# Optimization experiments

Hardware: AMD Instinct MI355X
Metric: run time of the kernel (lower is better)

## Reference

```python
import jax, jax.numpy as jnp
import numpy as np

N = 50000       # nodes
E = 800000      # edges (avg degree 16)
IN_DIM = 64
H = 64          # hidden_dim
OUT_DIM = 64
R = 8           # n_relations
L = 3           # n_layers
LN_EPS = 1e-5
NEG_SLOPE = 0.2


def _layer_norm(x, g, b):
    mu = jnp.mean(x, axis=-1, keepdims=True)
    var = jnp.mean((x - mu) ** 2, axis=-1, keepdims=True)
    return (x - mu) * jax.lax.rsqrt(var + LN_EPS) * g + b


def setup_inputs() -> dict:
    key = jax.random.key(0)
    ks = jax.random.split(key, 10)
    s = 0.05
    return {
        "x": jax.random.normal(ks[0], (N, IN_DIM), jnp.float32),
        "edge_index": jax.random.randint(ks[1], (2, E), 0, N),
        "edge_type": jax.random.randint(ks[2], (E,), 0, R),
        "W_in": jax.random.normal(ks[3], (H, IN_DIM), jnp.float32) * s,
        "b_in": jnp.zeros((H,), jnp.float32),
        "W_rel": jax.random.normal(ks[4], (R, H, H), jnp.float32) * s,   # no bias
        "W_gate": jax.random.normal(ks[5], (R, H, H), jnp.float32) * s,
        "b_gate": jnp.zeros((R, H), jnp.float32),
        "W_att": jax.random.normal(ks[6], (R, 2 * H), jnp.float32) * s,  # Linear(2H,1) per relation
        "b_att": jnp.zeros((R,), jnp.float32),
        "ln_gamma": jnp.ones((L, H), jnp.float32),
        "ln_beta": jnp.zeros((L, H), jnp.float32),
        "W_out": jax.random.normal(ks[7], (OUT_DIM, H), jnp.float32) * s,
        "b_out": jnp.zeros((OUT_DIM,), jnp.float32),
    }


def reference(x, edge_index, edge_type, W_in, b_in, W_rel, W_gate, b_gate,
              W_att, b_att, ln_gamma, ln_beta, W_out, b_out):
    src, dst = edge_index[0], edge_index[1]
    Wa_src, Wa_dst = W_att[:, :H], W_att[:, H:]      # [R,H] each
    seg = dst * R + edge_type                        # combined (node, relation) scatter key
    eidx = jnp.arange(E)

    h = jax.nn.relu(x @ W_in.T + b_in)               # [N,H]

    for layer in range(L):
        h_src = h[src]                               # [E,H] gather
        h_dst = h[dst]                               # [E,H] gather
        # attention score of each edge under its own relation's Linear(2H,1)
        scores_all = h_src @ Wa_src.T + h_dst @ Wa_dst.T + b_att   # [E,R]
        scores = scores_all[eidx, edge_type]                        # [E]
        scores = jax.nn.leaky_relu(scores, NEG_SLOPE)
        # softmax over dim=0 within each relation's edge set (as in the torch code)
        m = jax.ops.segment_max(scores, edge_type, num_segments=R)
        ex = jnp.exp(scores - m[edge_type])
        denom = jax.ops.segment_sum(ex, edge_type, num_segments=R)
        att = ex / denom[edge_type]                                 # [E]
        # relation-specific linear of source features (linear commutes with gather)
        hWr = jnp.einsum('nh,rkh->nrk', h, W_rel)                   # [N,R,H]
        msg = hWr[src, edge_type] * att[:, None]                    # [E,H]
        # per-relation scatter-add into destinations
        agg = jax.ops.segment_sum(msg, seg, num_segments=N * R)     # [N*R,H]
        agg = agg.reshape(N, R, H)
        gate = jax.nn.sigmoid(jnp.einsum('nh,rkh->nrk', h, W_gate) + b_gate)  # [N,R,H]
        h_new = jnp.mean(gate * agg, axis=1)         # sum(messages)/n_relations
        h = jax.nn.relu(_layer_norm(h + h_new, ln_gamma[layer], ln_beta[layer]))

    return h @ W_out.T + b_out
```

## Files before the change

### kernel.cpp

```cpp
#include <hip/hip_runtime.h>
#include <math.h>

#define NN 50000
#define EE 800000
#define HH 64
#define RR 8
#define LL 3
#define NR (NN * RR)
#define NB ((NR + 255) / 256)
#define LN_EPS 1e-5f
#define NEG_SLOPE 0.2f
#define LDH 68
#define OTB (16 * LDH)
#define DSPREAD 64
#define NPB 80
#define NGRP 5

typedef __attribute__((ext_vector_type(8))) short bf8;
typedef __attribute__((ext_vector_type(4))) float f4;
typedef __attribute__((ext_vector_type(2))) float f2;
typedef __attribute__((ext_vector_type(8))) unsigned short us8;
typedef __attribute__((ext_vector_type(2))) unsigned int u2;
typedef __attribute__((ext_vector_type(4))) unsigned int u4;

#define WLOADP(d0, d1, sbase, vbyte) \
    asm volatile("global_load_dwordx4 %0, %2, %3 offset:0\n\t" \
                 "global_load_dwordx4 %1, %2, %3 offset:64" \
        : "=&v"(d0), "=&v"(d1) : "v"(vbyte), "s"(sbase) : "memory")

__device__ __forceinline__ unsigned short bf16r(float f) {
    unsigned u = __float_as_uint(f);
    unsigned r = u + 0x7fffu + ((u >> 16) & 1u);
    return (unsigned short)(r >> 16);
}
__device__ __forceinline__ float bf2f(unsigned short u) {
    return __uint_as_float(((unsigned)u) << 16);
}
__device__ __forceinline__ bf8 asbf8(u4 v) {
    union { u4 a; bf8 b; } c; c.a = v; return c.b;
}
__device__ __forceinline__ void stage16(const void* g, void* l) {
    __builtin_amdgcn_global_load_lds(
        (const __attribute__((address_space(1))) void*)g,
        (__attribute__((address_space(3))) void*)l, 16, 0, 0);
}

__global__ __launch_bounds__(256) void proj_in(
    const float* __restrict__ x, const float* __restrict__ W,
    const float* __restrict__ bias, const unsigned short* __restrict__ WaB,
    float* __restrict__ h, unsigned short* __restrict__ hbf,
    float* __restrict__ s_src, float* __restrict__ s_dst) {
    __shared__ float WT[64 * LDH];
    __shared__ float xs[16 * LDH];
    __shared__ float hs[16 * LDH];
    int tid = threadIdx.x;
    int n0 = blockIdx.x * 16;
    #pragma unroll
    for (int s = 0; s < 16; ++s) {
        int idx = tid + 256 * s;
        int k = idx >> 6, i = idx & 63;
        WT[i * LDH + k] = W[idx];
    }
    int row = tid >> 4, cg = tid & 15;
    {
        f4 v = ((const f4*)x)[(size_t)(n0 + row) * 16 + cg];
        *(f4*)&xs[row * LDH + cg * 4] = v;
    }
    __syncthreads();
    f4 acc;
    {
        f4 b = *(const f4*)(bias + cg * 4);
        acc = b;
        #pragma unroll
        for (int i = 0; i < 64; ++i) {
            float xv = xs[row * LDH + i];
            f4 wt = *(const f4*)&WT[i * LDH + cg * 4];
            acc[0] += xv * wt[0];
            acc[1] += xv * wt[1];
            acc[2] += xv * wt[2];
            acc[3] += xv * wt[3];
        }
        #pragma unroll
        for (int j = 0; j < 4; ++j) acc[j] = fmaxf(acc[j], 0.f);
        int n = n0 + row;
        *(f4*)(h + (size_t)n * 64 + cg * 4) = acc;
        u2 u;
        u[0] = (unsigned)bf16r(acc[0]) | ((unsigned)bf16r(acc[1]) << 16);
        u[1] = (unsigned)bf16r(acc[2]) | ((unsigned)bf16r(acc[3]) << 16);
        *(u2*)(hbf + (size_t)n * 64 + cg * 4) = u;
        *(f4*)&hs[row * LDH + cg * 4] = acc;
    }
    __syncthreads();
    if (tid < 64) {
        int lane = tid;
        int quad = lane >> 4, lr = lane & 15;
        f4 sc = (f4){0.f, 0.f, 0.f, 0.f};
        #pragma unroll
        for (int kb = 0; kb < 2; ++kb) {
            const float* p = &hs[lr * LDH + kb * 32 + quad * 8];
            bf8 a;
            #pragma unroll
            for (int j = 0; j < 8; ++j) a[j] = (short)bf16r(p[j]);
            const bf8* bw = (const bf8*)(WaB + lr * 64 + kb * 32 + quad * 8);
            sc = __builtin_amdgcn_mfma_f32_16x16x32_bf16(a, *bw, sc, 0, 0, 0);
        }
        #pragma unroll
        for (int j = 0; j < 4; ++j) {
            int n = n0 + quad * 4 + j;
            if (lr < 8) s_src[n * 8 + lr] = sc[j];
            else        s_dst[n * 8 + (lr - 8)] = sc[j];
        }
    }
}

__global__ void edge_count(const int* __restrict__ ei, const int* __restrict__ et,
                           int* __restrict__ counts, int* __restrict__ rank) {
    int e = blockIdx.x * 256 + threadIdx.x;
    int d = ei[EE + e], t = et[e];
    rank[e] = atomicAdd(&counts[d * 8 + t], 1);
}

__global__ void scan1(const int* __restrict__ counts, int* __restrict__ offs,
                      int* __restrict__ bsum) {
    __shared__ int s[256];
    int tid = threadIdx.x;
    int i = blockIdx.x * 256 + tid;
    int v = (i < NR) ? counts[i] : 0;
    s[tid] = v; __syncthreads();
    for (int d = 1; d < 256; d <<= 1) {
        int x = (tid >= d) ? s[tid - d] : 0;
        __syncthreads();
        s[tid] += x;
        __syncthreads();
    }
    if (i < NR) offs[i] = s[tid] - v;
    if (tid == 255) bsum[blockIdx.x] = s[255];
}

__global__ void scan2(int* __restrict__ bsum) {
    __shared__ int s[1024];
    int tid = threadIdx.x;
    int carry = 0;
    for (int c0 = 0; c0 < NB; c0 += 1024) {
        int i = c0 + tid;
        int v = (i < NB) ? bsum[i] : 0;
        s[tid] = v; __syncthreads();
        for (int d = 1; d < 1024; d <<= 1) {
            int x = (tid >= d) ? s[tid - d] : 0;
            __syncthreads();
            s[tid] += x;
            __syncthreads();
        }
        if (i < NB) bsum[i] = carry + s[tid] - v;
        int tot = s[1023];
        __syncthreads();
        carry += tot;
    }
}

__global__ void edge_fill(const int* __restrict__ ei, const int* __restrict__ et,
                          const int* __restrict__ rank, const int* __restrict__ offs,
                          const int* __restrict__ bsum, u2* __restrict__ spack) {
    int e = blockIdx.x * 256 + threadIdx.x;
    int s = ei[e], d = ei[EE + e], t = et[e];
    int seg = d * 8 + t;
    int slot = offs[seg] + bsum[seg >> 8] + rank[e];
    spack[slot] = (u2){(unsigned)s, (unsigned)seg};
}

__global__ void cvt_w(const float* __restrict__ Wr, const float* __restrict__ Wg,
                      const float* __restrict__ Wa, const float* __restrict__ Wo,
                      unsigned short* __restrict__ WrB, unsigned short* __restrict__ WgB,
                      unsigned short* __restrict__ WaB, unsigned short* __restrict__ WoB) {
    int i = blockIdx.x * 256 + threadIdx.x;
    WrB[i] = bf16r(Wr[i]);
    WgB[i] = bf16r(Wg[i]);
    if (i < 1024) {
        int row = i >> 6, k = i & 63;
        float v = (row < 8) ? Wa[row * 128 + k] : Wa[(row - 8) * 128 + 64 + k];
        WaB[i] = bf16r(v);
    }
    if (i < 4096) WoB[i] = bf16r(Wo[i]);
}

__global__ void edge_softmax2(const u2* __restrict__ spack,
                              const float* __restrict__ s_src, const float* __restrict__ s_dst,
                              const float* __restrict__ b_att,
                              u2* __restrict__ epack, float* __restrict__ dpart) {
    __shared__ float lsum[4][8];
    int tid = threadIdx.x;
    if (tid < 32) lsum[tid >> 3][tid & 7] = 0.f;
    __syncthreads();
    int slot = blockIdx.x * 256 + tid;
    u2 sp = spack[slot];
    int src = (int)sp[0];
    int seg = (int)sp[1];
    int t = seg & 7;
    float sc = s_src[src * 8 + t] + s_dst[seg] + b_att[t];
    sc = (sc >= 0.f) ? sc : NEG_SLOPE * sc;
    float ex = __expf(sc);
    epack[slot] = (u2){(unsigned)src, __float_as_uint(ex)};
    atomicAdd(&lsum[tid >> 6][t], ex);
    __syncthreads();
    if (tid < 8) {
        float v = lsum[0][tid] + lsum[1][tid] + lsum[2][tid] + lsum[3][tid];
        atomicAdd(&dpart[(blockIdx.x & (DSPREAD - 1)) * 16 + tid], v);
    }
}

__global__ void denom_reduce(const float* __restrict__ dpartL,
                             float* __restrict__ idn8L) {
    __shared__ float sb[256];
    int t = threadIdx.x;
    int rb = t >> 3, ty = t & 7;
    float v = dpartL[rb * 16 + ty] + dpartL[(rb + 32) * 16 + ty];
    sb[t] = v; __syncthreads();
    for (int st = 128; st >= 8; st >>= 1) {
        if (t < st) sb[t] += sb[t + st];
        __syncthreads();
    }
    if (t < 8) idn8L[t] = 1.f / sb[t];
}

__global__ __launch_bounds__(256, 4) void gather_seg(
    const int* __restrict__ offs, const int* __restrict__ bsum,
    const u2* __restrict__ epack, const float* __restrict__ idn8L,
    const unsigned short* __restrict__ hbf_in,
    unsigned short* __restrict__ psG) {
    int tid = threadIdx.x;
    int segl = tid >> 1, half = tid & 1;
    int sidx = blockIdx.x * 128 + segl;
    int lo = offs[sidx] + bsum[sidx >> 8];
    int nxt = sidx + 1;
    int hi = (nxt < NR) ? (offs[nxt] + bsum[nxt >> 8]) : EE;
    int r = segl & 7, gn = segl >> 3;

    f4 d0 = *(const f4*)(idn8L);
    f4 d1 = *(const f4*)(idn8L + 4);
    float i01 = (r & 1) ? d0[1] : d0[0];
    float i23 = (r & 1) ? d0[3] : d0[2];
    float i45 = (r & 1) ? d1[1] : d1[0];
    float i67 = (r & 1) ? d1[3] : d1[2];
    float i03 = (r & 2) ? i23 : i01;
    float i47 = (r & 2) ? i67 : i45;
    float idn = (r & 4) ? i47 : i03;

    f2 acc[16];
    #pragma unroll
    for (int i = 0; i < 16; ++i) acc[i] = (f2){0.f, 0.f};

    for (int s = lo; s < hi; s += 4) {
        int i1 = (s + 1 < hi) ? s + 1 : s;
        int i2 = (s + 2 < hi) ? s + 2 : s;
        int i3 = (s + 3 < hi) ? s + 3 : s;
        u2 pk0 = epack[s], pk1 = epack[i1], pk2 = epack[i2], pk3 = epack[i3];
        float a0 = __uint_as_float(pk0[1]);
        float a1 = (s + 1 < hi) ? __uint_as_float(pk1[1]) : 0.f;
        float a2 = (s + 2 < hi) ? __uint_as_float(pk2[1]) : 0.f;
        float a3 = (s + 3 < hi) ? __uint_as_float(pk3[1]) : 0.f;
        const u4* hp0 = (const u4*)(hbf_in + ((size_t)(int)pk0[0] << 6) + half * 32);
        const u4* hp1 = (const u4*)(hbf_in + ((size_t)(int)pk1[0] << 6) + half * 32);
        const u4* hp2 = (const u4*)(hbf_in + ((size_t)(int)pk2[0] << 6) + half * 32);
        const u4* hp3 = (const u4*)(hbf_in + ((size_t)(int)pk3[0] << 6) + half * 32);
        #pragma unroll
        for (int q = 0; q < 4; ++q) {
            u4 v0 = hp0[q], v1 = hp1[q], v2 = hp2[q], v3 = hp3[q];
            #pragma unroll
            for (int k = 0; k < 4; ++k) {
                f2 w0, w1, w2, w3;
                w0[0] = __uint_as_float(v0[k] << 16);
                w0[1] = __uint_as_float(v0[k] & 0xffff0000u);
                w1[0] = __uint_as_float(v1[k] << 16);
                w1[1] = __uint_as_float(v1[k] & 0xffff0000u);
                w2[0] = __uint_as_float(v2[k] << 16);
                w2[1] = __uint_as_float(v2[k] & 0xffff0000u);
                w3[0] = __uint_as_float(v3[k] << 16);
                w3[1] = __uint_as_float(v3[k] & 0xffff0000u);
                acc[q * 4 + k] += (f2){a0, a0} * w0;
                acc[q * 4 + k] += (f2){a1, a1} * w1;
                acc[q * 4 + k] += (f2){a2, a2} * w2;
                acc[q * 4 + k] += (f2){a3, a3} * w3;
            }
        }
    }

    unsigned short* base = psG + ((size_t)blockIdx.x << 13) + gn * 512 + r * 64;
    #pragma unroll
    for (int q = 0; q < 4; ++q) {
        us8 o;
        #pragma unroll
        for (int k = 0; k < 4; ++k) {
            o[2 * k]     = bf16r(acc[q * 4 + k][0] * idn);
            o[2 * k + 1] = bf16r(acc[q * 4 + k][1] * idn);
        }
        int c2 = (half * 4 + q) ^ (gn & 7);
        *(us8*)(base + c2 * 8) = o;
    }
}

#define STAGE_GRP(b, g) do { \
    int n0s_ = nb0 + (g) * 16; \
    const char* ps_src_ = (const char*)psG + (size_t)n0s_ * 1024; \
    _Pragma("unroll") \
    for (int i_ = 0; i_ < 4; ++i_) { \
        unsigned off_ = i_ * 4096 + w * 1024; \
        stage16(ps_src_ + off_ + lane * 16, (char*)psL[b] + off_); \
    } \
    unsigned a_ = (unsigned)(w * 1024 + lane * 16); \
    unsigned sa_ = a_ ^ (((a_ >> 8) & 7u) << 4); \
    stage16((const char*)(hbuf + (size_t)n0s_ * 64) + sa_, (char*)hsL[b] + a_); \
} while (0)

template<bool EMIT, bool OUT>
__global__ __launch_bounds__(256, 2) void combine_dense(
    const float* __restrict__ hbuf, const unsigned short* __restrict__ psG,
    const unsigned short* __restrict__ WrB, const unsigned short* __restrict__ WgB,
    const unsigned short* __restrict__ WaB, const unsigned short* __restrict__ WoB,
    const float* __restrict__ b_gate, const float* __restrict__ gamma,
    const float* __restrict__ beta, float* __restrict__ hout,
    unsigned short* __restrict__ hbf_out, float* __restrict__ ssrc_out,
    float* __restrict__ sdst_out, float* __restrict__ outp,
    const float* __restrict__ b_out) {
    __shared__ unsigned short psL[2][8192];
    __shared__ float hsL[2][1024];
    int tid = threadIdx.x;
    int nb0 = blockIdx.x * NPB;
    int w = tid >> 6, lane = tid & 63;
    int quad = lane >> 4, lr = lane & 15;
    int tn = w;

    STAGE_GRP(0, 0);

    unsigned rowb = (unsigned)((tn * 16 + lr) * 128 + quad * 16);
    u4 wr[8][2], wg[8][2];
    #pragma unroll
    for (int r = 0; r < 8; ++r) {
        WLOADP(wr[r][0], wr[r][1], WrB, rowb + (unsigned)r * 8192u);
        WLOADP(wg[r][0], wg[r][1], WgB, rowb + (unsigned)r * 8192u);
    }
    float bgv[8];
    #pragma unroll
    for (int r = 0; r < 8; ++r) bgv[r] = b_gate[r * 64 + tn * 16 + lr];
    f4 gmv = *(const f4*)(gamma + (tid & 15) * 4);
    f4 btv = *(const f4*)(beta + (tid & 15) * 4);

    for (int g = 0; g < NGRP; ++g) {
        int cb = g & 1;
        int n0 = nb0 + g * 16;
        if (g + 1 < NGRP) {
            STAGE_GRP(cb ^ 1, g + 1);
            asm volatile("s_waitcnt vmcnt(5)" ::: "memory");
        } else {
            asm volatile("s_waitcnt vmcnt(0)" ::: "memory");
        }
        __builtin_amdgcn_sched_barrier(0);
        __builtin_amdgcn_s_barrier();

        bf8 a_h[2];
        #pragma unroll
        for (int kb = 0; kb < 2; ++kb) {
            unsigned c0 = (unsigned)(kb * 8 + quad * 2)     ^ (unsigned)(lr & 7);
            unsigned c1 = (unsigned)(kb * 8 + quad * 2 + 1) ^ (unsigned)(lr & 7);
            f4 p0 = *(const f4*)((const char*)hsL[cb] + lr * 256 + c0 * 16);
            f4 p1 = *(const f4*)((const char*)hsL[cb] + lr * 256 + c1 * 16);
            bf8 a;
            #pragma unroll
            for (int j = 0; j < 4; ++j) a[j] = (short)bf16r(p0[j]);
            #pragma unroll
            for (int j = 0; j < 4; ++j) a[4 + j] = (short)bf16r(p1[j]);
            a_h[kb] = a;
        }

        f4 acc = (f4){0.f, 0.f, 0.f, 0.f};
        #pragma unroll
        for (int r = 0; r < 8; ++r) {
            bf8 a_p[2];
            #pragma unroll
            for (int kb = 0; kb < 2; ++kb) {
                unsigned c = (unsigned)(kb * 4 + quad) ^ (unsigned)(lr & 7);
                a_p[kb] = *(const bf8*)((const char*)psL[cb] + lr * 1024 + r * 128 + c * 16);
            }
            f4 aggc = (f4){0.f, 0.f, 0.f, 0.f};
            f4 gacc = (f4){0.f, 0.f, 0.f, 0.f};
            aggc = __builtin_amdgcn_mfma_f32_16x16x32_bf16(a_p[0], asbf8(wr[r][0]), aggc, 0, 0, 0);
            gacc = __builtin_amdgcn_mfma_f32_16x16x32_bf16(a_h[0], asbf8(wg[r][0]), gacc, 0, 0, 0);
            aggc = __builtin_amdgcn_mfma_f32_16x16x32_bf16(a_p[1], asbf8(wr[r][1]), aggc, 0, 0, 0);
            gacc = __builtin_amdgcn_mfma_f32_16x16x32_bf16(a_h[1], asbf8(wg[r][1]), gacc, 0, 0, 0);
            #pragma unroll
            for (int j = 0; j < 4; ++j) {
                float gt = 1.f / (1.f + __expf(-(gacc[j] + bgv[r])));
                acc[j] += gt * aggc[j];
            }
        }
        __syncthreads();

        float* ps_f = (float*)psL[cb];
        #pragma unroll
        for (int j = 0; j < 4; ++j) {
            int row = quad * 4 + j;
            int col = tn * 16 + lr;
            unsigned y = (unsigned)(row * 256 + col * 4);
            float hres = *(const float*)((const char*)hsL[cb] + (y ^ (((unsigned)(row & 7)) << 4)));
            ps_f[row * LDH + col] = hres + acc[j] * 0.125f;
        }
        __syncthreads();

        {
            int row = tid >> 4, c = tid & 15;
            int n = n0 + row;
            f4 tv = *(const f4*)&ps_f[row * LDH + c * 4];
            float s1 = tv[0] + tv[1] + tv[2] + tv[3];
            float s2 = tv[0]*tv[0] + tv[1]*tv[1] + tv[2]*tv[2] + tv[3]*tv[3];
            #pragma unroll
            for (int off = 1; off <= 8; off <<= 1) {
                s1 += __shfl_xor(s1, off, 64);
                s2 += __shfl_xor(s2, off, 64);
            }
            float mu = s1 * (1.f / 64.f);
            float var = s2 * (1.f / 64.f) - mu * mu;
            float rs = rsqrtf(var + LN_EPS);
            f4 ov;
            #pragma unroll
            for (int j = 0; j < 4; ++j)
                ov[j] = fmaxf((tv[j] - mu) * rs * gmv[j] + btv[j], 0.f);
            if (!OUT)
                *(f4*)(hout + (size_t)n * 64 + c * 4) = ov;
            *(f4*)&ps_f[OTB + row * LDH + c * 4] = ov;
            if (EMIT) {
                u2 u;
                u[0] = (unsigned)bf16r(ov[0]) | ((unsigned)bf16r(ov[1]) << 16);
                u[1] = (unsigned)bf16r(ov[2]) | ((unsigned)bf16r(ov[3]) << 16);
                *(u2*)(hbf_out + (size_t)n * 64 + c * 4) = u;
            }
        }

        if (EMIT) {
            __syncthreads();
            if (w == 0) {
                f4 sc = (f4){0.f, 0.f, 0.f, 0.f};
                #pragma unroll
                for (int kb = 0; kb < 2; ++kb) {
                    const float* p = &ps_f[OTB + lr * LDH + kb * 32 + quad * 8];
                    bf8 a;
                    #pragma unroll
                    for (int j = 0; j < 8; ++j) a[j] = (short)bf16r(p[j]);
                    const bf8* bw = (const bf8*)(WaB + lr * 64 + kb * 32 + quad * 8);
                    sc = __builtin_amdgcn_mfma_f32_16x16x32_bf16(a, *bw, sc, 0, 0, 0);
                }
                #pragma unroll
                for (int j = 0; j < 4; ++j) {
                    int n = n0 + quad * 4 + j;
                    if (lr < 8) ssrc_out[n * 8 + lr] = sc[j];
                    else        sdst_out[n * 8 + (lr - 8)] = sc[j];
                }
            }
        }

        if (OUT) {
            __syncthreads();
            f4 oc = (f4){0.f, 0.f, 0.f, 0.f};
            #pragma unroll
            for (int kb = 0; kb < 2; ++kb) {
                const float* p = &ps_f[OTB + lr * LDH + kb * 32 + quad * 8];
                bf8 a;
                #pragma unroll
                for (int j = 0; j < 8; ++j) a[j] = (short)bf16r(p[j]);
                const bf8* bw = (const bf8*)(WoB + ((tn * 16 + lr) * 64 + kb * 32 + quad * 8));
                oc = __builtin_amdgcn_mfma_f32_16x16x32_bf16(a, *bw, oc, 0, 0, 0);
            }
            float bo = b_out[tn * 16 + lr];
            #pragma unroll
            for (int j = 0; j < 4; ++j)
                outp[(size_t)(n0 + quad * 4 + j) * 64 + tn * 16 + lr] = oc[j] + bo;
        }
        __syncthreads();
    }
}

extern "C" void kernel_launch(void* const* d_in, const int* in_sizes, int n_in,
                              void* d_out, int out_size, void* d_ws, size_t ws_size,
                              hipStream_t stream) {
    const float* x      = (const float*)d_in[0];
    const int*   ei     = (const int*)d_in[1];
    const int*   et     = (const int*)d_in[2];
    const float* W_in   = (const float*)d_in[3];
    const float* b_in   = (const float*)d_in[4];
    const float* W_rel  = (const float*)d_in[5];
    const float* W_gate = (const float*)d_in[6];
    const float* b_gate = (const float*)d_in[7];
    const float* W_att  = (const float*)d_in[8];
    const float* b_att  = (const float*)d_in[9];
    const float* ln_g   = (const float*)d_in[10];
    const float* ln_b   = (const float*)d_in[11];
    const float* W_out  = (const float*)d_in[12];
    const float* b_out  = (const float*)d_in[13];
    float* out = (float*)d_out;

    float* h0 = (float*)d_out;

    char* ws = (char*)d_ws;
    float* h1 = (float*)ws;                     ws += (size_t)NN * 64 * 4;
    unsigned short* hbfA = (unsigned short*)ws; ws += (size_t)NN * 64 * 2;
    unsigned short* hbfB = (unsigned short*)ws; ws += (size_t)NN * 64 * 2;
    float* s_src = (float*)ws;                  ws += (size_t)NN * 8 * 4;
    float* s_dst = (float*)ws;                  ws += (size_t)NN * 8 * 4;
    unsigned short* WrB = (unsigned short*)ws;  ws += (size_t)RR * 64 * 64 * 2;
    unsigned short* WgB = (unsigned short*)ws;  ws += (size_t)RR * 64 * 64 * 2;
    unsigned short* WaB = (unsigned short*)ws;  ws += 2048;
    unsigned short* WoB = (unsigned short*)ws;  ws += 8192;
    int* counts = (int*)ws;                     ws += (size_t)NR * 4;
    float* dpart = (float*)ws;                  ws += 3 * DSPREAD * 16 * 4;
    float* idn8G = (float*)ws;                  ws += 3 * 16 * 4;
    int* offs = (int*)ws;                       ws += (size_t)NR * 4;
    int* bsum = (int*)ws;                       ws += 6400;
    int* rank = (int*)ws;                       ws += (size_t)EE * 4;
    u2* spack = (u2*)ws;                        ws += (size_t)EE * 8;
    u2* epack = (u2*)ws;                        ws += (size_t)EE * 8;
    unsigned short* psG = (unsigned short*)ws;  ws += (size_t)NR * 64 * 2;

    hipMemsetAsync(counts, 0, (size_t)NR * 4 + 3 * DSPREAD * 16 * 4, stream);
    cvt_w<<<128, 256, 0, stream>>>(W_rel, W_gate, W_att, W_out, WrB, WgB, WaB, WoB);
    edge_count<<<EE / 256, 256, 0, stream>>>(ei, et, counts, rank);
    scan1<<<NB, 256, 0, stream>>>(counts, offs, bsum);
    scan2<<<1, 1024, 0, stream>>>(bsum);
    edge_fill<<<EE / 256, 256, 0, stream>>>(ei, et, rank, offs, bsum, spack);
    proj_in<<<NN / 16, 256, 0, stream>>>(x, W_in, b_in, WaB, h0, hbfA, s_src, s_dst);

    const int tiles16 = NN / 16;
    const int tiles80 = NN / NPB;
    float* hA = h0;  float* hB = h1;
    unsigned short* bfA = hbfA;  unsigned short* bfB = hbfB;
    for (int layer = 0; layer < LL; ++layer) {
        float* dpl = dpart + (size_t)layer * DSPREAD * 16;
        float* idn = idn8G + (size_t)layer * 16;
        edge_softmax2<<<EE / 256, 256, 0, stream>>>(spack, s_src, s_dst, b_att,
                                                    epack, dpl);
        denom_reduce<<<1, 256, 0, stream>>>(dpl, idn);
        gather_seg<<<tiles16, 256, 0, stream>>>(offs, bsum, epack, idn, bfA, psG);
        if (layer < LL - 1) {
            combine_dense<true, false><<<tiles80, 256, 0, stream>>>(
                hA, psG, WrB, WgB, WaB, WoB, b_gate,
                ln_g + layer * 64, ln_b + layer * 64,
                hB, bfB, s_src, s_dst, out, b_out);
        } else {
            combine_dense<false, true><<<tiles80, 256, 0, stream>>>(
                hA, psG, WrB, WgB, WaB, WoB, b_gate,
                ln_g + layer * 64, ln_b + layer * 64,
                hB, bfB, s_src, s_dst, out, b_out);
        }
        float* tf = hA; hA = hB; hB = tf;
        unsigned short* tb = bfA; bfA = bfB; bfB = tb;
    }
}
```

Before: 413.5 us.

## Fuse edge softmax into segment gather and defer denominator to combine

Removes the separate edge_softmax2 kernel and the epack buffer. The gather kernel now computes each edge's leaky-relu score and its exponential inline, and accumulates per-relation exponential sums into dpart. The division by the global per-relation denominator moves into combine_dense, which is valid because the denominator is constant per relation. This removes one kernel launch and a full write and read of the per-edge buffer each layer. In exchange the gather does extra exp work and loads from s_src, and unnormalized partial sums are rounded to bf16 before scaling.

```diff
diff --git a/kernel.cpp b/kernel.cpp
--- a/kernel.cpp
+++ b/kernel.cpp
@@ -183,31 +183,6 @@
     if (i < 4096) WoB[i] = bf16r(Wo[i]);
 }
 
-__global__ void edge_softmax2(const u2* __restrict__ spack,
-                              const float* __restrict__ s_src, const float* __restrict__ s_dst,
-                              const float* __restrict__ b_att,
-                              u2* __restrict__ epack, float* __restrict__ dpart) {
-    __shared__ float lsum[4][8];
-    int tid = threadIdx.x;
-    if (tid < 32) lsum[tid >> 3][tid & 7] = 0.f;
-    __syncthreads();
-    int slot = blockIdx.x * 256 + tid;
-    u2 sp = spack[slot];
-    int src = (int)sp[0];
-    int seg = (int)sp[1];
-    int t = seg & 7;
-    float sc = s_src[src * 8 + t] + s_dst[seg] + b_att[t];
-    sc = (sc >= 0.f) ? sc : NEG_SLOPE * sc;
-    float ex = __expf(sc);
-    epack[slot] = (u2){(unsigned)src, __float_as_uint(ex)};
-    atomicAdd(&lsum[tid >> 6][t], ex);
-    __syncthreads();
-    if (tid < 8) {
-        float v = lsum[0][tid] + lsum[1][tid] + lsum[2][tid] + lsum[3][tid];
-        atomicAdd(&dpart[(blockIdx.x & (DSPREAD - 1)) * 16 + tid], v);
-    }
-}
-
 __global__ void denom_reduce(const float* __restrict__ dpartL,
                              float* __restrict__ idn8L) {
     __shared__ float sb[256];
@@ -224,9 +199,10 @@
 
 __global__ __launch_bounds__(256, 4) void gather_seg(
     const int* __restrict__ offs, const int* __restrict__ bsum,
-    const u2* __restrict__ epack, const float* __restrict__ idn8L,
+    const u2* __restrict__ spack, const float* __restrict__ s_src,
+    const float* __restrict__ s_dst, const float* __restrict__ b_att,
     const unsigned short* __restrict__ hbf_in,
-    unsigned short* __restrict__ psG) {
+    unsigned short* __restrict__ psG, float* __restrict__ dpart) {
     int tid = threadIdx.x;
     int segl = tid >> 1, half = tid & 1;
     int sidx = blockIdx.x * 128 + segl;
@@ -235,33 +211,37 @@
     int hi = (nxt < NR) ? (offs[nxt] + bsum[nxt >> 8]) : EE;
     int r = segl & 7, gn = segl >> 3;
 
-    f4 d0 = *(const f4*)(idn8L);
-    f4 d1 = *(const f4*)(idn8L + 4);
-    float i01 = (r & 1) ? d0[1] : d0[0];
-    float i23 = (r & 1) ? d0[3] : d0[2];
-    float i45 = (r & 1) ? d1[1] : d1[0];
-    float i67 = (r & 1) ? d1[3] : d1[2];
-    float i03 = (r & 2) ? i23 : i01;
-    float i47 = (r & 2) ? i67 : i45;
-    float idn = (r & 4) ? i47 : i03;
+    float bconst = s_dst[sidx] + b_att[r];
 
     f2 acc[16];
     #pragma unroll
     for (int i = 0; i < 16; ++i) acc[i] = (f2){0.f, 0.f};
+    float exsum = 0.f;
 
     for (int s = lo; s < hi; s += 4) {
         int i1 = (s + 1 < hi) ? s + 1 : s;
         int i2 = (s + 2 < hi) ? s + 2 : s;
         int i3 = (s + 3 < hi) ? s + 3 : s;
-        u2 pk0 = epack[s], pk1 = epack[i1], pk2 = epack[i2], pk3 = epack[i3];
-        float a0 = __uint_as_float(pk0[1]);
-        float a1 = (s + 1 < hi) ? __uint_as_float(pk1[1]) : 0.f;
-        float a2 = (s + 2 < hi) ? __uint_as_float(pk2[1]) : 0.f;
-        float a3 = (s + 3 < hi) ? __uint_as_float(pk3[1]) : 0.f;
-        const u4* hp0 = (const u4*)(hbf_in + ((size_t)(int)pk0[0] << 6) + half * 32);
-        const u4* hp1 = (const u4*)(hbf_in + ((size_t)(int)pk1[0] << 6) + half * 32);
-        const u4* hp2 = (const u4*)(hbf_in + ((size_t)(int)pk2[0] << 6) + half * 32);
-        const u4* hp3 = (const u4*)(hbf_in + ((size_t)(int)pk3[0] << 6) + half * 32);
+        u2 sp0 = spack[s], sp1 = spack[i1], sp2 = spack[i2], sp3 = spack[i3];
+        int sr0 = (int)sp0[0], sr1 = (int)sp1[0];
+        int sr2 = (int)sp2[0], sr3 = (int)sp3[0];
+        float sc0 = s_src[sr0 * 8 + r] + bconst;
+        float sc1 = s_src[sr1 * 8 + r] + bconst;
+        float sc2 = s_src[sr2 * 8 + r] + bconst;
+        float sc3 = s_src[sr3 * 8 + r] + bconst;
+        sc0 = (sc0 >= 0.f) ? sc0 : NEG_SLOPE * sc0;
+        sc1 = (sc1 >= 0.f) ? sc1 : NEG_SLOPE * sc1;
+        sc2 = (sc2 >= 0.f) ? sc2 : NEG_SLOPE * sc2;
+        sc3 = (sc3 >= 0.f) ? sc3 : NEG_SLOPE * sc3;
+        float a0 = __expf(sc0);
+        float a1 = (s + 1 < hi) ? __expf(sc1) : 0.f;
+        float a2 = (s + 2 < hi) ? __expf(sc2) : 0.f;
+        float a3 = (s + 3 < hi) ? __expf(sc3) : 0.f;
+        exsum += a0 + a1 + a2 + a3;
+        const u4* hp0 = (const u4*)(hbf_in + ((size_t)sr0 << 6) + half * 32);
+        const u4* hp1 = (const u4*)(hbf_in + ((size_t)sr1 << 6) + half * 32);
+        const u4* hp2 = (const u4*)(hbf_in + ((size_t)sr2 << 6) + half * 32);
+        const u4* hp3 = (const u4*)(hbf_in + ((size_t)sr3 << 6) + half * 32);
         #pragma unroll
         for (int q = 0; q < 4; ++q) {
             u4 v0 = hp0[q], v1 = hp1[q], v2 = hp2[q], v3 = hp3[q];
@@ -284,14 +264,24 @@
         }
     }
 
+    {
+        float v = half ? 0.f : exsum;
+        v += __shfl_xor(v, 1, 64);
+        v += __shfl_xor(v, 16, 64);
+        v += __shfl_xor(v, 32, 64);
+        int lane = tid & 63;
+        if ((lane & 1) == 0 && lane < 16)
+            atomicAdd(&dpart[(blockIdx.x & (DSPREAD - 1)) * 16 + ((lane >> 1) & 7)], v);
+    }
+
     unsigned short* base = psG + ((size_t)blockIdx.x << 13) + gn * 512 + r * 64;
     #pragma unroll
     for (int q = 0; q < 4; ++q) {
         us8 o;
         #pragma unroll
         for (int k = 0; k < 4; ++k) {
-            o[2 * k]     = bf16r(acc[q * 4 + k][0] * idn);
-            o[2 * k + 1] = bf16r(acc[q * 4 + k][1] * idn);
+            o[2 * k]     = bf16r(acc[q * 4 + k][0]);
+            o[2 * k + 1] = bf16r(acc[q * 4 + k][1]);
         }
         int c2 = (half * 4 + q) ^ (gn & 7);
         *(us8*)(base + c2 * 8) = o;
@@ -314,6 +304,7 @@
 template<bool EMIT, bool OUT>
 __global__ __launch_bounds__(256, 2) void combine_dense(
     const float* __restrict__ hbuf, const unsigned short* __restrict__ psG,
+    const float* __restrict__ idn8L,
     const unsigned short* __restrict__ WrB, const unsigned short* __restrict__ WgB,
     const unsigned short* __restrict__ WaB, const unsigned short* __restrict__ WoB,
     const float* __restrict__ b_gate, const float* __restrict__ gamma,
@@ -343,6 +334,10 @@
     for (int r = 0; r < 8; ++r) bgv[r] = b_gate[r * 64 + tn * 16 + lr];
     f4 gmv = *(const f4*)(gamma + (tid & 15) * 4);
     f4 btv = *(const f4*)(beta + (tid & 15) * 4);
+    f4 id0 = *(const f4*)idn8L;
+    f4 id1 = *(const f4*)(idn8L + 4);
+    float idnv[8] = {id0[0], id0[1], id0[2], id0[3],
+                     id1[0], id1[1], id1[2], id1[3]};
 
     for (int g = 0; g < NGRP; ++g) {
         int cb = g & 1;
@@ -389,7 +384,7 @@
             #pragma unroll
             for (int j = 0; j < 4; ++j) {
                 float gt = 1.f / (1.f + __expf(-(gacc[j] + bgv[r])));
-                acc[j] += gt * aggc[j];
+                acc[j] += gt * (aggc[j] * idnv[r]);
             }
         }
         __syncthreads();
@@ -515,7 +510,6 @@
     int* bsum = (int*)ws;                       ws += 6400;
     int* rank = (int*)ws;                       ws += (size_t)EE * 4;
     u2* spack = (u2*)ws;                        ws += (size_t)EE * 8;
-    u2* epack = (u2*)ws;                        ws += (size_t)EE * 8;
     unsigned short* psG = (unsigned short*)ws;  ws += (size_t)NR * 64 * 2;
 
     hipMemsetAsync(counts, 0, (size_t)NR * 4 + 3 * DSPREAD * 16 * 4, stream);
@@ -533,18 +527,17 @@
     for (int layer = 0; layer < LL; ++layer) {
         float* dpl = dpart + (size_t)layer * DSPREAD * 16;
         float* idn = idn8G + (size_t)layer * 16;
-        edge_softmax2<<<EE / 256, 256, 0, stream>>>(spack, s_src, s_dst, b_att,
-                                                    epack, dpl);
+        gather_seg<<<tiles16, 256, 0, stream>>>(offs, bsum, spack, s_src, s_dst,
+                                                b_att, bfA, psG, dpl);
         denom_reduce<<<1, 256, 0, stream>>>(dpl, idn);
-        gather_seg<<<tiles16, 256, 0, stream>>>(offs, bsum, epack, idn, bfA, psG);
         if (layer < LL - 1) {
             combine_dense<true, false><<<tiles80, 256, 0, stream>>>(
-                hA, psG, WrB, WgB, WaB, WoB, b_gate,
+                hA, psG, idn, WrB, WgB, WaB, WoB, b_gate,
                 ln_g + layer * 64, ln_b + layer * 64,
                 hB, bfB, s_src, s_dst, out, b_out);
         } else {
             combine_dense<false, true><<<tiles80, 256, 0, stream>>>(
-                hA, psG, WrB, WgB, WaB, WoB, b_gate,
+                hA, psG, idn, WrB, WgB, WaB, WoB, b_gate,
                 ln_g + layer * 64, ln_b + layer * 64,
                 hB, bfB, s_src, s_dst, out, b_out);
         }
```

New measurement: 412.8 us. No clear change (-0.2%).
